# Performance work log

Hardware: AMD Instinct MI355X
Metric: run time of the kernel (lower is better)

The kernel has to match this reference:

```python
import jax, jax.numpy as jnp
import numpy as np

B, S, D = 4, 2048, 2048
H, HD = 16, 128
ROPE_THETA = 10000.0


def rotate_half(x):
    half = x.shape[-1] // 2
    return jnp.concatenate([-x[..., half:], x[..., :half]], axis=-1)


def setup_inputs() -> dict:
    key = jax.random.key(0)
    ks = jax.random.split(key, 5)
    scale = 1.0 / np.sqrt(D)
    x = jax.random.normal(ks[0], (B, S, D), dtype=jnp.float32)
    wq = jax.random.normal(ks[1], (D, H * HD), dtype=jnp.float32) * scale
    wk = jax.random.normal(ks[2], (D, H * HD), dtype=jnp.float32) * scale
    wv = jax.random.normal(ks[3], (D, H * HD), dtype=jnp.float32) * scale
    wo = jax.random.normal(ks[4], (H * HD, D), dtype=jnp.float32) * scale
    # RoPE frequencies: freqs_cis real/imag parts, shape [S, HD//2]
    inv_freq = 1.0 / (ROPE_THETA ** (np.arange(0, HD, 2, dtype=np.float32) / HD))
    t = np.arange(S, dtype=np.float32)
    freqs = np.outer(t, inv_freq)  # [S, HD//2]
    cos = jnp.asarray(np.cos(freqs), dtype=jnp.float32)
    sin = jnp.asarray(np.sin(freqs), dtype=jnp.float32)
    return {"x": x, "wq": wq, "wk": wk, "wv": wv, "wo": wo, "cos": cos, "sin": sin}


def reference(x, wq, wk, wv, wo, cos, sin):
    batch, seq_len, _ = x.shape
    # QKV projections (no bias), reshape to [b, h, s, d]
    q = (x @ wq).reshape(batch, seq_len, H, HD).transpose(0, 2, 1, 3)
    k = (x @ wk).reshape(batch, seq_len, H, HD).transpose(0, 2, 1, 3)
    v = (x @ wv).reshape(batch, seq_len, H, HD)  # [b, s, h, d]
    # RoPE (half-split / rotate_half convention)
    cos_full = jnp.concatenate([cos, cos], axis=-1)[None, None, :seq_len, :]
    sin_full = jnp.concatenate([sin, sin], axis=-1)[None, None, :seq_len, :]
    q = q * cos_full + rotate_half(q) * sin_full
    k = k * cos_full + rotate_half(k) * sin_full
    # Scaled dot-product attention with causal mask
    logits = jnp.einsum('bhqd,bhkd->bhqk', q, k) / jnp.sqrt(jnp.float32(HD))
    causal = jnp.tril(jnp.ones((seq_len, seq_len), dtype=bool))
    logits = jnp.where(causal[None, None, :, :], logits, -1e10)
    weights = jax.nn.softmax(logits, axis=-1)
    out = jnp.einsum('bhqk,bkhd->bqhd', weights, v)
    out = out.reshape(batch, seq_len, H * HD)
    return out @ wo
```

## Files before the change

### kernel.cpp

```cpp
#include <hip/hip_runtime.h>
#include <cstdint>
#include <cstddef>

typedef unsigned short u16;
using bf16x8  = __attribute__((ext_vector_type(8))) short;
using floatx4 = __attribute__((ext_vector_type(4))) float;

__device__ __forceinline__ u16 f2bf(float f) {
    union { float f; unsigned u; } v; v.f = f;
    unsigned r = v.u + 0x7fffu + ((v.u >> 16) & 1u);
    return (u16)(r >> 16);
}
__device__ __forceinline__ float bf2f(u16 h) {
    union { unsigned u; float f; } v; v.u = ((unsigned)h) << 16; return v.f;
}
__device__ __forceinline__ floatx4 mfma16(bf16x8 a, bf16x8 b, floatx4 c) {
    return __builtin_amdgcn_mfma_f32_16x16x32_bf16(a, b, c, 0, 0, 0);
}
using gptr_t = const __attribute__((address_space(1))) unsigned int*;
using lptr_t = __attribute__((address_space(3))) unsigned int*;
__device__ __forceinline__ void lds16(const void* g, void* l) {
    __builtin_amdgcn_global_load_lds((gptr_t)g, (lptr_t)l, 16, 0, 0);
}

#define ATT_SCALE 0.1275758218522532f

__global__ __launch_bounds__(256) void cvt_x(const float* __restrict__ x, u16* __restrict__ xb) {
    size_t i = ((size_t)blockIdx.x * 256 + threadIdx.x) * 4;
    float4 v = *(const float4*)&x[i];
    ushort4 r; r.x = f2bf(v.x); r.y = f2bf(v.y); r.z = f2bf(v.z); r.w = f2bf(v.w);
    *(ushort4*)&xb[i] = r;
}

__global__ __launch_bounds__(256) void transpose_w(const float* __restrict__ in, u16* __restrict__ out) {
    __shared__ float t[64][65];
    int k0 = blockIdx.x * 64, n0 = blockIdx.y * 64;
    int tx = threadIdx.x, ty = threadIdx.y;
#pragma unroll
    for (int i = 0; i < 16; ++i) {
        int r = i * 4 + ty;
        t[r][tx] = in[(size_t)(k0 + r) * 2048 + n0 + tx];
    }
    __syncthreads();
#pragma unroll
    for (int i = 0; i < 16; ++i) {
        int r = i * 4 + ty;
        out[(size_t)(n0 + r) * 2048 + k0 + tx] = f2bf(t[tx][r]);
    }
}

template <int MODE>
__global__ __launch_bounds__(256) void gemm_bt(const u16* __restrict__ A, const u16* __restrict__ B,
                                               u16* __restrict__ Qo, u16* __restrict__ Ko, u16* __restrict__ Vo,
                                               float* __restrict__ Co) {
    __shared__ __align__(16) u16 As[128 * 64];
    __shared__ __align__(16) u16 Bs[128 * 64];
    const int m0 = blockIdx.y << 7;
    const int n0 = blockIdx.x << 7;
    const int tid = threadIdx.x;
    const int w = tid >> 6, lane = tid & 63;
    const int wm = w >> 1, wn = w & 1;
    const int m16 = lane & 15, q4 = lane >> 4;

    floatx4 acc[4][4];
#pragma unroll
    for (int r = 0; r < 4; ++r)
#pragma unroll
        for (int c = 0; c < 4; ++c) acc[r][c] = (floatx4)0.0f;

    const u16* Abase = A + (size_t)(m0 + w * 32 + (lane >> 3)) * 2048 + (lane & 7) * 8;
    const u16* Bbase = B + (size_t)(n0 + w * 32 + (lane >> 3)) * 2048 + (lane & 7) * 8;
    u16* lA = As + (w * 32) * 64;
    u16* lB = Bs + (w * 32) * 64;

    for (int kt = 0; kt < 32; ++kt) {
        __syncthreads();
        const u16* ga = Abase + kt * 64;
        const u16* gb = Bbase + kt * 64;
#pragma unroll
        for (int t = 0; t < 4; ++t) {
            lds16(ga + (size_t)t * 8 * 2048, lA + t * 8 * 64);
            lds16(gb + (size_t)t * 8 * 2048, lB + t * 8 * 64);
        }
        __syncthreads();
#pragma unroll
        for (int kk = 0; kk < 2; ++kk) {
            bf16x8 af[4], bfr[4];
#pragma unroll
            for (int r = 0; r < 4; ++r)
                af[r] = *(const bf16x8*)&As[(wm * 64 + r * 16 + m16) * 64 + kk * 32 + q4 * 8];
#pragma unroll
            for (int c = 0; c < 4; ++c)
                bfr[c] = *(const bf16x8*)&Bs[(wn * 64 + c * 16 + m16) * 64 + kk * 32 + q4 * 8];
#pragma unroll
            for (int r = 0; r < 4; ++r)
#pragma unroll
                for (int c = 0; c < 4; ++c)
                    acc[r][c] = mfma16(af[r], bfr[c], acc[r][c]);
        }
    }

    if (MODE == 0) {
        const int which = n0 >> 11;
        const int h = (n0 >> 7) & 15;
        u16* dst = (which == 0) ? Qo : ((which == 1) ? Ko : Vo);
#pragma unroll
        for (int r = 0; r < 4; ++r) {
#pragma unroll
            for (int c = 0; c < 4; ++c) {
                int d = wn * 64 + c * 16 + m16;
                int mbase = m0 + wm * 64 + r * 16 + q4 * 4;
#pragma unroll
                for (int i = 0; i < 4; ++i) {
                    int mm = mbase + i;
                    int b = mm >> 11, s = mm & 2047;
                    dst[((size_t)((b * 16 + h) * 2048 + s) << 7) + d] = f2bf(acc[r][c][i]);
                }
            }
        }
    } else {
#pragma unroll
        for (int r = 0; r < 4; ++r) {
#pragma unroll
            for (int c = 0; c < 4; ++c) {
                int n = n0 + wn * 64 + c * 16 + m16;
                int mbase = m0 + wm * 64 + r * 16 + q4 * 4;
#pragma unroll
                for (int i = 0; i < 4; ++i)
                    Co[(size_t)(mbase + i) * 2048 + n] = acc[r][c][i];
            }
        }
    }
}

__global__ __launch_bounds__(256) void rope_qk(u16* __restrict__ Q, u16* __restrict__ K,
                                               const float* __restrict__ cosb, const float* __restrict__ sinb) {
    int t = blockIdx.x * 256 + threadIdx.x;
    int d = t & 63;
    int row = t >> 6;
    int s = row & 2047;
    float c = cosb[s * 64 + d], sn = sinb[s * 64 + d];
    size_t base = (size_t)row * 128;
    float q0 = bf2f(Q[base + d]), q1 = bf2f(Q[base + 64 + d]);
    Q[base + d]      = f2bf((q0 * c - q1 * sn) * ATT_SCALE);
    Q[base + 64 + d] = f2bf((q1 * c + q0 * sn) * ATT_SCALE);
    float k0 = bf2f(K[base + d]), k1 = bf2f(K[base + 64 + d]);
    K[base + d]      = f2bf(k0 * c - k1 * sn);
    K[base + 64 + d] = f2bf(k1 * c + k0 * sn);
}

__global__ __launch_bounds__(256) void transpose_v(const u16* __restrict__ V, u16* __restrict__ VT) {
    __shared__ u16 t[64][65];
    int bh = blockIdx.z;
    const u16* in = V + (size_t)bh * 2048 * 128;
    u16* out = VT + (size_t)bh * 128 * 2048;
    int s0 = blockIdx.x * 64, d0 = blockIdx.y * 64;
    int tx = threadIdx.x, ty = threadIdx.y;
#pragma unroll
    for (int i = 0; i < 16; ++i) {
        int r = i * 4 + ty;
        t[r][tx] = in[(size_t)(s0 + r) * 128 + d0 + tx];
    }
    __syncthreads();
#pragma unroll
    for (int i = 0; i < 16; ++i) {
        int r = i * 4 + ty;
        out[(size_t)(d0 + r) * 2048 + s0 + tx] = t[tx][r];
    }
}

__global__ __launch_bounds__(512, 4) void attn_kernel(const u16* __restrict__ Q, const u16* __restrict__ K,
                                                      const u16* __restrict__ VT, u16* __restrict__ AO) {
    __shared__ __align__(16) u16 ks[64 * 136];
    __shared__ __align__(16) u16 vts[128 * 72];
    __shared__ __align__(16) u16 ps[128 * 72];
    const int bx = blockIdx.x;
    const int iq = 15 - (bx >> 6);
    const int bh = bx & 63;
    const int b = bh >> 4, h = bh & 15;
    const u16* Qg = Q  + (size_t)bh * (2048 * 128);
    const u16* Kg = K  + (size_t)bh * (2048 * 128);
    const u16* Vg = VT + (size_t)bh * (128 * 2048);
    const int tid = threadIdx.x, w = tid >> 6, lane = tid & 63;
    const int m16 = lane & 15, q4 = lane >> 4;

    const int qrow = iq * 128 + w * 16;
    bf16x8 qf[4];
#pragma unroll
    for (int kk = 0; kk < 4; ++kk)
        qf[kk] = *(const bf16x8*)&Qg[(size_t)(qrow + m16) * 128 + kk * 32 + q4 * 8];

    floatx4 o[8];
#pragma unroll
    for (int c = 0; c < 8; ++c) o[c] = (floatx4)0.0f;
    float mrow = -1e30f, lrow = 0.0f;

    const int jn = 2 * iq + 2;
    for (int j = 0; j < jn; ++j) {
        __syncthreads();
        {
            int u0 = tid, u1 = tid + 512;
            int r0 = u0 >> 4, c0 = u0 & 15, r1 = u1 >> 4, c1 = u1 & 15;
            uint4 ka = *(const uint4*)&Kg[(size_t)(j * 64 + r0) * 128 + c0 * 8];
            uint4 kb2 = *(const uint4*)&Kg[(size_t)(j * 64 + r1) * 128 + c1 * 8];
            int vr0 = tid >> 3, vc0 = tid & 7, vr1 = (tid + 512) >> 3, vc1 = tid & 7;
            uint4 va = *(const uint4*)&Vg[(size_t)vr0 * 2048 + j * 64 + vc0 * 8];
            uint4 vb2 = *(const uint4*)&Vg[(size_t)vr1 * 2048 + j * 64 + vc1 * 8];
            *(uint4*)&ks[r0 * 136 + c0 * 8] = ka;
            *(uint4*)&ks[r1 * 136 + c1 * 8] = kb2;
            *(uint4*)&vts[vr0 * 72 + vc0 * 8] = va;
            *(uint4*)&vts[vr1 * 72 + vc1 * 8] = vb2;
        }
        __syncthreads();

        floatx4 sacc[4];
#pragma unroll
        for (int r = 0; r < 4; ++r) sacc[r] = (floatx4)0.0f;
#pragma unroll
        for (int kk = 0; kk < 4; ++kk) {
            bf16x8 kb[4];
#pragma unroll
            for (int r = 0; r < 4; ++r)
                kb[r] = *(const bf16x8*)&ks[(r * 16 + m16) * 136 + kk * 32 + q4 * 8];
#pragma unroll
            for (int r = 0; r < 4; ++r)
                sacc[r] = mfma16(kb[r], qf[kk], sacc[r]);
        }

        if (j >= 2 * iq) {
            const int qg = qrow + m16;
#pragma unroll
            for (int r = 0; r < 4; ++r)
#pragma unroll
                for (int i = 0; i < 4; ++i) {
                    int kg = j * 64 + r * 16 + q4 * 4 + i;
                    if (kg > qg) sacc[r][i] = -1e30f;
                }
        }

        float pmax = -1e30f;
#pragma unroll
        for (int r = 0; r < 4; ++r)
#pragma unroll
            for (int i = 0; i < 4; ++i) pmax = fmaxf(pmax, sacc[r][i]);
        pmax = fmaxf(pmax, __shfl_xor(pmax, 16));
        pmax = fmaxf(pmax, __shfl_xor(pmax, 32));
        float mnew = fmaxf(mrow, pmax);
        float alpha = __builtin_amdgcn_exp2f(mrow - mnew);
        mrow = mnew;

        float psum = 0.0f;
#pragma unroll
        for (int r = 0; r < 4; ++r) {
            float p0 = __builtin_amdgcn_exp2f(sacc[r][0] - mnew);
            float p1 = __builtin_amdgcn_exp2f(sacc[r][1] - mnew);
            float p2 = __builtin_amdgcn_exp2f(sacc[r][2] - mnew);
            float p3 = __builtin_amdgcn_exp2f(sacc[r][3] - mnew);
            psum += (p0 + p1) + (p2 + p3);
            ushort4 pk; pk.x = f2bf(p0); pk.y = f2bf(p1); pk.z = f2bf(p2); pk.w = f2bf(p3);
            *(ushort4*)&ps[(w * 16 + m16) * 72 + r * 16 + q4 * 4] = pk;
        }
        psum += __shfl_xor(psum, 16);
        psum += __shfl_xor(psum, 32);
        lrow = lrow * alpha + psum;

        float abc[4];
#pragma unroll
        for (int i = 0; i < 4; ++i) abc[i] = __shfl(alpha, q4 * 4 + i);
#pragma unroll
        for (int c = 0; c < 8; ++c)
#pragma unroll
            for (int i = 0; i < 4; ++i) o[c][i] *= abc[i];

#pragma unroll
        for (int kk = 0; kk < 2; ++kk) {
            bf16x8 pa = *(const bf16x8*)&ps[(w * 16 + m16) * 72 + kk * 32 + q4 * 8];
            bf16x8 vb[8];
#pragma unroll
            for (int c = 0; c < 8; ++c)
                vb[c] = *(const bf16x8*)&vts[(c * 16 + m16) * 72 + kk * 32 + q4 * 8];
#pragma unroll
            for (int c = 0; c < 8; ++c)
                o[c] = mfma16(pa, vb[c], o[c]);
        }
    }

    float linv = __builtin_amdgcn_rcpf(lrow);
    float li[4];
#pragma unroll
    for (int i = 0; i < 4; ++i) li[i] = __shfl(linv, q4 * 4 + i);
#pragma unroll
    for (int c = 0; c < 8; ++c)
#pragma unroll
        for (int i = 0; i < 4; ++i) {
            int s = qrow + q4 * 4 + i;
            int d = c * 16 + m16;
            AO[((size_t)(b * 2048 + s)) * 2048 + h * 128 + d] = f2bf(o[c][i] * li[i]);
        }
}

extern "C" void kernel_launch(void* const* d_in, const int* in_sizes, int n_in,
                              void* d_out, int out_size, void* d_ws, size_t ws_size,
                              hipStream_t stream) {
    const float* x    = (const float*)d_in[0];
    const float* wq   = (const float*)d_in[1];
    const float* wk   = (const float*)d_in[2];
    const float* wv   = (const float*)d_in[3];
    const float* wo   = (const float*)d_in[4];
    const float* cosb = (const float*)d_in[5];
    const float* sinb = (const float*)d_in[6];
    float* out = (float*)d_out;

    char* ws = (char*)d_ws;
    u16* xb    = (u16*)(ws);
    u16* AO    = xb;
    u16* wqkvb = (u16*)(ws + 33554432);
    u16* wob   = (u16*)(ws + 58720256);
    u16* Qb    = (u16*)(ws + 67108864);
    u16* Kb    = (u16*)(ws + 100663296);
    u16* Vb    = (u16*)(ws + 134217728);
    u16* Vtb   = (u16*)(ws + 167772160);

    cvt_x<<<16384, 256, 0, stream>>>(x, xb);
    transpose_w<<<dim3(32, 32), dim3(64, 4), 0, stream>>>(wq, wqkvb);
    transpose_w<<<dim3(32, 32), dim3(64, 4), 0, stream>>>(wk, wqkvb + (size_t)2048 * 2048);
    transpose_w<<<dim3(32, 32), dim3(64, 4), 0, stream>>>(wv, wqkvb + (size_t)2 * 2048 * 2048);
    transpose_w<<<dim3(32, 32), dim3(64, 4), 0, stream>>>(wo, wob);

    gemm_bt<0><<<dim3(48, 64), 256, 0, stream>>>(xb, wqkvb, Qb, Kb, Vb, nullptr);
    rope_qk<<<32768, 256, 0, stream>>>(Qb, Kb, cosb, sinb);
    transpose_v<<<dim3(32, 2, 64), dim3(64, 4), 0, stream>>>(Vb, Vtb);
    attn_kernel<<<1024, 512, 0, stream>>>(Qb, Kb, Vtb, AO);
    gemm_bt<1><<<dim3(16, 64), 256, 0, stream>>>(AO, wob, nullptr, nullptr, nullptr, out);
}
```

Measured before the change: 652.5 us.

## Fuse RoPE into QKV GEMM epilogue, merge weight transposes, restructure attention tiles

The separate RoPE kernel is removed: the QKV GEMM permutes its N-column mapping so each wave holds both rotary halves and applies RoPE and the attention scale in its epilogue. The four weight-transpose launches are merged into one 3D grid. The attention kernel moves to 256 threads with 32 query rows per wave and double-buffers K in LDS through a register prefetch. V fragments are now read straight from global memory instead of being staged in LDS. This saves a full read/write pass over Q and K and some launch overhead, but adds register pressure and uncoalesced global V reads in the attention inner loop.

```diff
diff --git a/kernel.cpp b/kernel.cpp
--- a/kernel.cpp
+++ b/kernel.cpp
@@ -32,8 +32,13 @@
     *(ushort4*)&xb[i] = r;
 }
 
-__global__ __launch_bounds__(256) void transpose_w(const float* __restrict__ in, u16* __restrict__ out) {
+__global__ __launch_bounds__(256) void transpose_wall(const float* __restrict__ wq, const float* __restrict__ wk,
+                                                      const float* __restrict__ wv, const float* __restrict__ wo,
+                                                      u16* __restrict__ wqkvb, u16* __restrict__ wob) {
     __shared__ float t[64][65];
+    const int z = blockIdx.z;
+    const float* in = (z == 0) ? wq : (z == 1) ? wk : (z == 2) ? wv : wo;
+    u16* out = (z < 3) ? (wqkvb + (size_t)z * 2048 * 2048) : wob;
     int k0 = blockIdx.x * 64, n0 = blockIdx.y * 64;
     int tx = threadIdx.x, ty = threadIdx.y;
 #pragma unroll
@@ -52,7 +57,8 @@
 template <int MODE>
 __global__ __launch_bounds__(256) void gemm_bt(const u16* __restrict__ A, const u16* __restrict__ B,
                                                u16* __restrict__ Qo, u16* __restrict__ Ko, u16* __restrict__ Vo,
-                                               float* __restrict__ Co) {
+                                               float* __restrict__ Co,
+                                               const float* __restrict__ cosb, const float* __restrict__ sinb) {
     __shared__ __align__(16) u16 As[128 * 64];
     __shared__ __align__(16) u16 Bs[128 * 64];
     const int m0 = blockIdx.y << 7;
@@ -62,6 +68,12 @@
     const int wm = w >> 1, wn = w & 1;
     const int m16 = lane & 15, q4 = lane >> 4;
 
+    int nsel[4];
+#pragma unroll
+    for (int c = 0; c < 4; ++c)
+        nsel[c] = (MODE == 0) ? ((c >> 1) * 64 + wn * 32 + ((c & 1) << 4) + m16)
+                              : (wn * 64 + c * 16 + m16);
+
     floatx4 acc[4][4];
 #pragma unroll
     for (int r = 0; r < 4; ++r)
@@ -91,7 +103,7 @@
                 af[r] = *(const bf16x8*)&As[(wm * 64 + r * 16 + m16) * 64 + kk * 32 + q4 * 8];
 #pragma unroll
             for (int c = 0; c < 4; ++c)
-                bfr[c] = *(const bf16x8*)&Bs[(wn * 64 + c * 16 + m16) * 64 + kk * 32 + q4 * 8];
+                bfr[c] = *(const bf16x8*)&Bs[nsel[c] * 64 + kk * 32 + q4 * 8];
 #pragma unroll
             for (int r = 0; r < 4; ++r)
 #pragma unroll
@@ -104,17 +116,38 @@
         const int which = n0 >> 11;
         const int h = (n0 >> 7) & 15;
         u16* dst = (which == 0) ? Qo : ((which == 1) ? Ko : Vo);
-#pragma unroll
-        for (int r = 0; r < 4; ++r) {
-#pragma unroll
-            for (int c = 0; c < 4; ++c) {
-                int d = wn * 64 + c * 16 + m16;
-                int mbase = m0 + wm * 64 + r * 16 + q4 * 4;
+        if (which < 2) {
+            const float sc = (which == 0) ? ATT_SCALE : 1.0f;
+#pragma unroll
+            for (int r = 0; r < 4; ++r) {
 #pragma unroll
                 for (int i = 0; i < 4; ++i) {
-                    int mm = mbase + i;
+                    int mm = m0 + wm * 64 + r * 16 + q4 * 4 + i;
                     int b = mm >> 11, s = mm & 2047;
-                    dst[((size_t)((b * 16 + h) * 2048 + s) << 7) + d] = f2bf(acc[r][c][i]);
+                    size_t rowbase = ((size_t)((b * 16 + h) * 2048 + s)) << 7;
+#pragma unroll
+                    for (int cp = 0; cp < 2; ++cp) {
+                        int d63 = wn * 32 + cp * 16 + m16;
+                        float cs = cosb[s * 64 + d63], sn = sinb[s * 64 + d63];
+                        float lo = acc[r][cp][i], hi = acc[r][cp + 2][i];
+                        dst[rowbase + d63]      = f2bf((lo * cs - hi * sn) * sc);
+                        dst[rowbase + d63 + 64] = f2bf((hi * cs + lo * sn) * sc);
+                    }
+                }
+            }
+        } else {
+#pragma unroll
+            for (int r = 0; r < 4; ++r) {
+#pragma unroll
+                for (int c = 0; c < 4; ++c) {
+                    int d = (c >> 1) * 64 + wn * 32 + ((c & 1) << 4) + m16;
+                    int mbase = m0 + wm * 64 + r * 16 + q4 * 4;
+#pragma unroll
+                    for (int i = 0; i < 4; ++i) {
+                        int mm = mbase + i;
+                        int b = mm >> 11, s = mm & 2047;
+                        dst[((size_t)((b * 16 + h) * 2048 + s) << 7) + d] = f2bf(acc[r][c][i]);
+                    }
                 }
             }
         }
@@ -131,22 +164,6 @@
             }
         }
     }
-}
-
-__global__ __launch_bounds__(256) void rope_qk(u16* __restrict__ Q, u16* __restrict__ K,
-                                               const float* __restrict__ cosb, const float* __restrict__ sinb) {
-    int t = blockIdx.x * 256 + threadIdx.x;
-    int d = t & 63;
-    int row = t >> 6;
-    int s = row & 2047;
-    float c = cosb[s * 64 + d], sn = sinb[s * 64 + d];
-    size_t base = (size_t)row * 128;
-    float q0 = bf2f(Q[base + d]), q1 = bf2f(Q[base + 64 + d]);
-    Q[base + d]      = f2bf((q0 * c - q1 * sn) * ATT_SCALE);
-    Q[base + 64 + d] = f2bf((q1 * c + q0 * sn) * ATT_SCALE);
-    float k0 = bf2f(K[base + d]), k1 = bf2f(K[base + 64 + d]);
-    K[base + d]      = f2bf(k0 * c - k1 * sn);
-    K[base + 64 + d] = f2bf(k1 * c + k0 * sn);
 }
 
 __global__ __launch_bounds__(256) void transpose_v(const u16* __restrict__ V, u16* __restrict__ VT) {
@@ -169,10 +186,9 @@
     }
 }
 
-__global__ __launch_bounds__(512, 4) void attn_kernel(const u16* __restrict__ Q, const u16* __restrict__ K,
+__global__ __launch_bounds__(256, 2) void attn_kernel(const u16* __restrict__ Q, const u16* __restrict__ K,
                                                       const u16* __restrict__ VT, u16* __restrict__ AO) {
-    __shared__ __align__(16) u16 ks[64 * 136];
-    __shared__ __align__(16) u16 vts[128 * 72];
+    __shared__ __align__(16) u16 ks[2][64 * 136];
     __shared__ __align__(16) u16 ps[128 * 72];
     const int bx = blockIdx.x;
     const int iq = 15 - (bx >> 6);
@@ -183,120 +199,162 @@
     const u16* Vg = VT + (size_t)bh * (128 * 2048);
     const int tid = threadIdx.x, w = tid >> 6, lane = tid & 63;
     const int m16 = lane & 15, q4 = lane >> 4;
-
-    const int qrow = iq * 128 + w * 16;
-    bf16x8 qf[4];
-#pragma unroll
-    for (int kk = 0; kk < 4; ++kk)
-        qf[kk] = *(const bf16x8*)&Qg[(size_t)(qrow + m16) * 128 + kk * 32 + q4 * 8];
-
-    floatx4 o[8];
-#pragma unroll
-    for (int c = 0; c < 8; ++c) o[c] = (floatx4)0.0f;
-    float mrow = -1e30f, lrow = 0.0f;
-
     const int jn = 2 * iq + 2;
+
+    const int qrow = iq * 128 + w * 32;
+    bf16x8 qf[2][4];
+#pragma unroll
+    for (int rm = 0; rm < 2; ++rm)
+#pragma unroll
+        for (int kk = 0; kk < 4; ++kk)
+            qf[rm][kk] = *(const bf16x8*)&Qg[(size_t)(qrow + rm * 16 + m16) * 128 + kk * 32 + q4 * 8];
+
+    floatx4 o[2][8];
+#pragma unroll
+    for (int rm = 0; rm < 2; ++rm)
+#pragma unroll
+        for (int c = 0; c < 8; ++c) o[rm][c] = (floatx4)0.0f;
+    float mrow[2] = {-1e30f, -1e30f}, lrow[2] = {0.0f, 0.0f};
+
+    uint4 kreg[4];
+#pragma unroll
+    for (int u = 0; u < 4; ++u) {
+        int id = u * 256 + tid;
+        kreg[u] = *(const uint4*)&Kg[(size_t)(id >> 4) * 128 + (id & 15) * 8];
+    }
+    {
+#pragma unroll
+        for (int u = 0; u < 4; ++u) {
+            int id = u * 256 + tid;
+            *(uint4*)&ks[0][(id >> 4) * 136 + (id & 15) * 8] = kreg[u];
+        }
+        int j1 = (1 < jn) ? 1 : 0;
+#pragma unroll
+        for (int u = 0; u < 4; ++u) {
+            int id = u * 256 + tid;
+            kreg[u] = *(const uint4*)&Kg[(size_t)(j1 * 64 + (id >> 4)) * 128 + (id & 15) * 8];
+        }
+    }
+    __syncthreads();
+
     for (int j = 0; j < jn; ++j) {
-        __syncthreads();
-        {
-            int u0 = tid, u1 = tid + 512;
-            int r0 = u0 >> 4, c0 = u0 & 15, r1 = u1 >> 4, c1 = u1 & 15;
-            uint4 ka = *(const uint4*)&Kg[(size_t)(j * 64 + r0) * 128 + c0 * 8];
-            uint4 kb2 = *(const uint4*)&Kg[(size_t)(j * 64 + r1) * 128 + c1 * 8];
-            int vr0 = tid >> 3, vc0 = tid & 7, vr1 = (tid + 512) >> 3, vc1 = tid & 7;
-            uint4 va = *(const uint4*)&Vg[(size_t)vr0 * 2048 + j * 64 + vc0 * 8];
-            uint4 vb2 = *(const uint4*)&Vg[(size_t)vr1 * 2048 + j * 64 + vc1 * 8];
-            *(uint4*)&ks[r0 * 136 + c0 * 8] = ka;
-            *(uint4*)&ks[r1 * 136 + c1 * 8] = kb2;
-            *(uint4*)&vts[vr0 * 72 + vc0 * 8] = va;
-            *(uint4*)&vts[vr1 * 72 + vc1 * 8] = vb2;
-        }
-        __syncthreads();
-
-        floatx4 sacc[4];
-#pragma unroll
-        for (int r = 0; r < 4; ++r) sacc[r] = (floatx4)0.0f;
+        const int cur = j & 1;
+        if (j + 1 < jn) {
+#pragma unroll
+            for (int u = 0; u < 4; ++u) {
+                int id = u * 256 + tid;
+                *(uint4*)&ks[1 - cur][(id >> 4) * 136 + (id & 15) * 8] = kreg[u];
+            }
+            int j2 = (j + 2 < jn) ? (j + 2) : (jn - 1);
+#pragma unroll
+            for (int u = 0; u < 4; ++u) {
+                int id = u * 256 + tid;
+                kreg[u] = *(const uint4*)&Kg[(size_t)(j2 * 64 + (id >> 4)) * 128 + (id & 15) * 8];
+            }
+        }
+
+        floatx4 sacc[2][4];
+#pragma unroll
+        for (int rm = 0; rm < 2; ++rm)
+#pragma unroll
+            for (int r = 0; r < 4; ++r) sacc[rm][r] = (floatx4)0.0f;
 #pragma unroll
         for (int kk = 0; kk < 4; ++kk) {
             bf16x8 kb[4];
 #pragma unroll
             for (int r = 0; r < 4; ++r)
-                kb[r] = *(const bf16x8*)&ks[(r * 16 + m16) * 136 + kk * 32 + q4 * 8];
+                kb[r] = *(const bf16x8*)&ks[cur][(r * 16 + m16) * 136 + kk * 32 + q4 * 8];
+#pragma unroll
+            for (int rm = 0; rm < 2; ++rm)
+#pragma unroll
+                for (int r = 0; r < 4; ++r)
+                    sacc[rm][r] = mfma16(kb[r], qf[rm][kk], sacc[rm][r]);
+        }
+
+        if (j >= 2 * iq) {
+#pragma unroll
+            for (int rm = 0; rm < 2; ++rm) {
+                const int qg = qrow + rm * 16 + m16;
+#pragma unroll
+                for (int r = 0; r < 4; ++r)
+#pragma unroll
+                    for (int i = 0; i < 4; ++i) {
+                        int kg = j * 64 + r * 16 + q4 * 4 + i;
+                        if (kg > qg) sacc[rm][r][i] = -1e30f;
+                    }
+            }
+        }
+
+#pragma unroll
+        for (int rm = 0; rm < 2; ++rm) {
+            float pmax = -1e30f;
 #pragma unroll
             for (int r = 0; r < 4; ++r)
-                sacc[r] = mfma16(kb[r], qf[kk], sacc[r]);
-        }
-
-        if (j >= 2 * iq) {
-            const int qg = qrow + m16;
-#pragma unroll
-            for (int r = 0; r < 4; ++r)
-#pragma unroll
-                for (int i = 0; i < 4; ++i) {
-                    int kg = j * 64 + r * 16 + q4 * 4 + i;
-                    if (kg > qg) sacc[r][i] = -1e30f;
-                }
-        }
-
-        float pmax = -1e30f;
-#pragma unroll
-        for (int r = 0; r < 4; ++r)
-#pragma unroll
-            for (int i = 0; i < 4; ++i) pmax = fmaxf(pmax, sacc[r][i]);
-        pmax = fmaxf(pmax, __shfl_xor(pmax, 16));
-        pmax = fmaxf(pmax, __shfl_xor(pmax, 32));
-        float mnew = fmaxf(mrow, pmax);
-        float alpha = __builtin_amdgcn_exp2f(mrow - mnew);
-        mrow = mnew;
-
-        float psum = 0.0f;
-#pragma unroll
-        for (int r = 0; r < 4; ++r) {
-            float p0 = __builtin_amdgcn_exp2f(sacc[r][0] - mnew);
-            float p1 = __builtin_amdgcn_exp2f(sacc[r][1] - mnew);
-            float p2 = __builtin_amdgcn_exp2f(sacc[r][2] - mnew);
-            float p3 = __builtin_amdgcn_exp2f(sacc[r][3] - mnew);
-            psum += (p0 + p1) + (p2 + p3);
-            ushort4 pk; pk.x = f2bf(p0); pk.y = f2bf(p1); pk.z = f2bf(p2); pk.w = f2bf(p3);
-            *(ushort4*)&ps[(w * 16 + m16) * 72 + r * 16 + q4 * 4] = pk;
-        }
-        psum += __shfl_xor(psum, 16);
-        psum += __shfl_xor(psum, 32);
-        lrow = lrow * alpha + psum;
-
-        float abc[4];
-#pragma unroll
-        for (int i = 0; i < 4; ++i) abc[i] = __shfl(alpha, q4 * 4 + i);
+#pragma unroll
+                for (int i = 0; i < 4; ++i) pmax = fmaxf(pmax, sacc[rm][r][i]);
+            pmax = fmaxf(pmax, __shfl_xor(pmax, 16));
+            pmax = fmaxf(pmax, __shfl_xor(pmax, 32));
+            float mnew = fmaxf(mrow[rm], pmax);
+            float alpha = __builtin_amdgcn_exp2f(mrow[rm] - mnew);
+            mrow[rm] = mnew;
+
+            float psum = 0.0f;
+#pragma unroll
+            for (int r = 0; r < 4; ++r) {
+                float p0 = __builtin_amdgcn_exp2f(sacc[rm][r][0] - mnew);
+                float p1 = __builtin_amdgcn_exp2f(sacc[rm][r][1] - mnew);
+                float p2 = __builtin_amdgcn_exp2f(sacc[rm][r][2] - mnew);
+                float p3 = __builtin_amdgcn_exp2f(sacc[rm][r][3] - mnew);
+                psum += (p0 + p1) + (p2 + p3);
+                ushort4 pk; pk.x = f2bf(p0); pk.y = f2bf(p1); pk.z = f2bf(p2); pk.w = f2bf(p3);
+                *(ushort4*)&ps[(w * 32 + rm * 16 + m16) * 72 + r * 16 + q4 * 4] = pk;
+            }
+            psum += __shfl_xor(psum, 16);
+            psum += __shfl_xor(psum, 32);
+            lrow[rm] = lrow[rm] * alpha + psum;
+
+            float abc[4];
+#pragma unroll
+            for (int i = 0; i < 4; ++i) abc[i] = __shfl(alpha, q4 * 4 + i);
+#pragma unroll
+            for (int c = 0; c < 8; ++c)
+#pragma unroll
+                for (int i = 0; i < 4; ++i) o[rm][c][i] *= abc[i];
+        }
+
+#pragma unroll
+        for (int kk = 0; kk < 2; ++kk) {
+            bf16x8 pa[2], vb[8];
+#pragma unroll
+            for (int rm = 0; rm < 2; ++rm)
+                pa[rm] = *(const bf16x8*)&ps[(w * 32 + rm * 16 + m16) * 72 + kk * 32 + q4 * 8];
+#pragma unroll
+            for (int c = 0; c < 8; ++c)
+                vb[c] = *(const bf16x8*)&Vg[(size_t)(c * 16 + m16) * 2048 + j * 64 + kk * 32 + q4 * 8];
+#pragma unroll
+            for (int rm = 0; rm < 2; ++rm)
+#pragma unroll
+                for (int c = 0; c < 8; ++c)
+                    o[rm][c] = mfma16(pa[rm], vb[c], o[rm][c]);
+        }
+        __syncthreads();
+    }
+
+#pragma unroll
+    for (int rm = 0; rm < 2; ++rm) {
+        float linv = __builtin_amdgcn_rcpf(lrow[rm]);
+        float li[4];
+#pragma unroll
+        for (int i = 0; i < 4; ++i) li[i] = __shfl(linv, q4 * 4 + i);
 #pragma unroll
         for (int c = 0; c < 8; ++c)
 #pragma unroll
-            for (int i = 0; i < 4; ++i) o[c][i] *= abc[i];
-
-#pragma unroll
-        for (int kk = 0; kk < 2; ++kk) {
-            bf16x8 pa = *(const bf16x8*)&ps[(w * 16 + m16) * 72 + kk * 32 + q4 * 8];
-            bf16x8 vb[8];
-#pragma unroll
-            for (int c = 0; c < 8; ++c)
-                vb[c] = *(const bf16x8*)&vts[(c * 16 + m16) * 72 + kk * 32 + q4 * 8];
-#pragma unroll
-            for (int c = 0; c < 8; ++c)
-                o[c] = mfma16(pa, vb[c], o[c]);
-        }
-    }
-
-    float linv = __builtin_amdgcn_rcpf(lrow);
-    float li[4];
-#pragma unroll
-    for (int i = 0; i < 4; ++i) li[i] = __shfl(linv, q4 * 4 + i);
-#pragma unroll
-    for (int c = 0; c < 8; ++c)
-#pragma unroll
-        for (int i = 0; i < 4; ++i) {
-            int s = qrow + q4 * 4 + i;
-            int d = c * 16 + m16;
-            AO[((size_t)(b * 2048 + s)) * 2048 + h * 128 + d] = f2bf(o[c][i] * li[i]);
-        }
+            for (int i = 0; i < 4; ++i) {
+                int s = qrow + rm * 16 + q4 * 4 + i;
+                int d = c * 16 + m16;
+                AO[((size_t)(b * 2048 + s)) * 2048 + h * 128 + d] = f2bf(o[rm][c][i] * li[i]);
+            }
+    }
 }
 
 extern "C" void kernel_launch(void* const* d_in, const int* in_sizes, int n_in,
@@ -322,14 +380,10 @@
     u16* Vtb   = (u16*)(ws + 167772160);
 
     cvt_x<<<16384, 256, 0, stream>>>(x, xb);
-    transpose_w<<<dim3(32, 32), dim3(64, 4), 0, stream>>>(wq, wqkvb);
-    transpose_w<<<dim3(32, 32), dim3(64, 4), 0, stream>>>(wk, wqkvb + (size_t)2048 * 2048);
-    transpose_w<<<dim3(32, 32), dim3(64, 4), 0, stream>>>(wv, wqkvb + (size_t)2 * 2048 * 2048);
-    transpose_w<<<dim3(32, 32), dim3(64, 4), 0, stream>>>(wo, wob);
-
-    gemm_bt<0><<<dim3(48, 64), 256, 0, stream>>>(xb, wqkvb, Qb, Kb, Vb, nullptr);
-    rope_qk<<<32768, 256, 0, stream>>>(Qb, Kb, cosb, sinb);
+    transpose_wall<<<dim3(32, 32, 4), dim3(64, 4), 0, stream>>>(wq, wk, wv, wo, wqkvb, wob);
+
+    gemm_bt<0><<<dim3(48, 64), 256, 0, stream>>>(xb, wqkvb, Qb, Kb, Vb, nullptr, cosb, sinb);
     transpose_v<<<dim3(32, 2, 64), dim3(64, 4), 0, stream>>>(Vb, Vtb);
-    attn_kernel<<<1024, 512, 0, stream>>>(Qb, Kb, Vtb, AO);
-    gemm_bt<1><<<dim3(16, 64), 256, 0, stream>>>(AO, wob, nullptr, nullptr, nullptr, out);
-}
+    attn_kernel<<<1024, 256, 0, stream>>>(Qb, Kb, Vtb, AO);
+    gemm_bt<1><<<dim3(16, 64), 256, 0, stream>>>(AO, wob, nullptr, nullptr, nullptr, out, cosb, sinb);
+}
```

New measurement: 773.9 us. +18.6%, slower.
